# Optimization experiments

Hardware: AMD Instinct MI355X
Metric: run time of the kernel (lower is better)

## Reference

```python
import jax, jax.numpy as jnp
import numpy as np
import math

N, C, H = 2048, 256, 8
D = C // H
T, R, E = 8, 12, 32768
BUCKETS = 21
SEED = 128


def _layernorm(x, g, b, eps=1e-5):
    mu = jnp.mean(x, axis=-1, keepdims=True)
    var = jnp.var(x, axis=-1, keepdims=True)
    return (x - mu) * jax.lax.rsqrt(var + eps) * g + b


def _bucketize_dt(dt, num_buckets):
    eps = 1e-06
    signed_log = jnp.sign(dt) * jnp.log1p(jnp.abs(dt) + eps)
    min_v, max_v = -5.0, 5.0
    norm = (jnp.clip(signed_log, min_v, max_v) - min_v) / (max_v - min_v + 1e-09)
    idx = jnp.floor(norm * (num_buckets - 1)).astype(jnp.int32)
    return jnp.clip(idx, 0, num_buckets - 1)


def setup_inputs() -> dict:
    key = jax.random.key(0)
    ks = jax.random.split(key, 24)
    s = 0.02
    inp = {
        'X': jax.random.normal(ks[0], (N, C), jnp.float32),
        'token_type': jax.random.randint(ks[1], (N,), 0, T, jnp.int32),
        'edge_src': jax.random.randint(ks[2], (E,), 0, N, jnp.int32),
        'edge_dst': jax.random.randint(ks[3], (E,), 0, N, jnp.int32),
        'edge_rel': jax.random.randint(ks[4], (E,), 0, R, jnp.int32),
        'time_vec': jax.random.normal(ks[5], (N,), jnp.float32),
        'seed_count': SEED,
        'Wq': jax.random.normal(ks[6], (C, C), jnp.float32) * s,
        'bq': jnp.zeros((C,), jnp.float32),
        'Wk': jax.random.normal(ks[7], (C, C), jnp.float32) * s,
        'bk': jnp.zeros((C,), jnp.float32),
        'Wv': jax.random.normal(ks[8], (C, C), jnp.float32) * s,
        'bv': jnp.zeros((C,), jnp.float32),
        'Wo': jax.random.normal(ks[9], (C, C), jnp.float32) * s,
        'bo': jnp.zeros((C,), jnp.float32),
        'ln1_g': jnp.ones((C,), jnp.float32),
        'ln1_b': jnp.zeros((C,), jnp.float32),
        'ln2_g': jnp.ones((C,), jnp.float32),
        'ln2_b': jnp.zeros((C,), jnp.float32),
        'W1': jax.random.normal(ks[10], (C, 4 * C), jnp.float32) * s,
        'b1': jnp.zeros((4 * C,), jnp.float32),
        'W2': jax.random.normal(ks[11], (4 * C, C), jnp.float32) * s,
        'b2': jnp.zeros((C,), jnp.float32),
        'adj_rel_bias': jnp.zeros((R, H), jnp.float32),
        'typepair_bias': jnp.zeros((T, T, H), jnp.float32),
        'temp_bias': jax.random.normal(ks[12], (BUCKETS, H), jnp.float32) * s,
    }
    return inp


def reference(X, token_type, edge_src, edge_dst, edge_rel, time_vec, seed_count,
              Wq, bq, Wk, bk, Wv, bv, Wo, bo,
              ln1_g, ln1_b, ln2_g, ln2_b, W1, b1, W2, b2,
              adj_rel_bias, typepair_bias, temp_bias):
    n = X.shape[0]
    h = _layernorm(X, ln1_g, ln1_b)
    q = (h @ Wq + bq).reshape(n, H, D)
    k = (h @ Wk + bk).reshape(n, H, D)
    v = (h @ Wv + bv).reshape(n, H, D)
    scores = jnp.einsum('nhd,mhd->hnm', q, k) / math.sqrt(D)  # [H, N, N]

    # structural bias, factored as [N, N, H] then transposed
    bias = typepair_bias[token_type][:, token_type]            # [N, N, H]
    bias = bias.at[edge_src, edge_dst].add(adj_rel_bias[edge_rel])
    # seed-wise temporal bias on the first seed_count rows
    dt = time_vec[None, :] - time_vec[:seed_count, None]       # [S, N]
    tb = temp_bias[_bucketize_dt(dt, BUCKETS)]                 # [S, N, H]
    bias = bias.at[:seed_count].add(tb)

    attn = jax.nn.softmax(scores + bias.transpose(2, 0, 1), axis=-1)
    o = jnp.einsum('hnm,mhd->nhd', attn, v).reshape(n, C)
    x = X + (o @ Wo + bo)

    h2 = _layernorm(x, ln2_g, ln2_b)
    f = jax.nn.gelu(h2 @ W1 + b1, approximate=False) @ W2 + b2
    return x + f
```

## Files before the change

### kernel.cpp

```cpp
#include <hip/hip_runtime.h>
#include <hip/hip_bf16.h>
#include <math.h>

#define NTOK 2048
#define CDIM 256
#define HHEADS 8
#define DHEAD 32
#define NEDGE 32768
#define NTILE2 32
#define EXTD 64
#define LE 72
#define LP3 144

typedef __attribute__((ext_vector_type(8))) short short8;
typedef __attribute__((ext_vector_type(4))) short short4v;
typedef __attribute__((ext_vector_type(4))) float f32x4;

static __device__ inline short f2bf(float f) {
    __hip_bfloat16 h = __float2bfloat16(f);
    return *reinterpret_cast<short*>(&h);
}
static __device__ inline float bf2f(short s) {
    unsigned int u = ((unsigned int)(unsigned short)s) << 16;
    return *reinterpret_cast<float*>(&u);
}
static __device__ inline unsigned char f2fp8(float f) {
    int pk = __builtin_amdgcn_cvt_pk_fp8_f32(f, f, 0, false);
    return (unsigned char)(pk & 0xFF);
}

static __device__ inline void transpose_tile_f32(const float* __restrict__ in,
    short* __restrict__ out, int K, int N, int k0, int n0, int t)
{
    __shared__ float tile[64][65];
    int r0 = t >> 4, c0 = (t & 15) * 4;
    #pragma unroll
    for (int i = 0; i < 4; i++) {
        int r = r0 + i * 16;
        float4 v = *(const float4*)(in + (size_t)(k0 + r) * N + n0 + c0);
        tile[r][c0 + 0] = v.x; tile[r][c0 + 1] = v.y;
        tile[r][c0 + 2] = v.z; tile[r][c0 + 3] = v.w;
    }
    __syncthreads();
    #pragma unroll
    for (int i = 0; i < 4; i++) {
        int nr = r0 + i * 16;
        short o4[4];
        #pragma unroll
        for (int j = 0; j < 4; j++) o4[j] = f2bf(tile[c0 + j][nr]);
        *(short4v*)(out + (size_t)(n0 + nr) * K + k0 + c0) = *(short4v*)o4;
    }
}

__global__ __launch_bounds__(256) void prep_kernel(
    const float* __restrict__ Wq, const float* __restrict__ Wk,
    const float* __restrict__ Wv, const float* __restrict__ Wo,
    const float* __restrict__ W1, const float* __restrict__ W2,
    short* __restrict__ wt_qkv, short* __restrict__ wot,
    short* __restrict__ w1t, short* __restrict__ w2t,
    const int* __restrict__ token_type, const float* __restrict__ typepair_bias,
    short* __restrict__ qh, short* __restrict__ kh,
    int* __restrict__ cnt2, float* __restrict__ rowsum,
    const float* __restrict__ X, const float* __restrict__ ln1_g,
    const float* __restrict__ ln1_b, short* __restrict__ h1)
{
    int b = blockIdx.x;
    int t = threadIdx.x;
    if (b < 192) {
        const float* src; short* dst; int K, N, bx, by;
        if (b < 64) {
            int m = b >> 4, r = b & 15;
            src = (m == 0) ? Wq : (m == 1) ? Wk : (m == 2) ? Wv : Wo;
            dst = (m == 0) ? wt_qkv : (m == 1) ? wt_qkv + 256 * 256
                : (m == 2) ? wt_qkv + 512 * 256 : wot;
            K = 256; N = 256; bx = r & 3; by = r >> 2;
        } else if (b < 128) {
            int r = b - 64; src = W1; dst = w1t; K = 256; N = 1024; bx = r & 15; by = r >> 4;
        } else {
            int r = b - 128; src = W2; dst = w2t; K = 1024; N = 256; bx = r & 3; by = r >> 2;
        }
        transpose_tile_f32(src, dst, K, N, by * 64, bx * 64, t);
    } else if (b < 256) {
        int idx = (b - 192) * 256 + t;
        int row = idx >> 3, h = idx & 7;
        int tt = token_type[row];
        short qe[32], ke[32];
        #pragma unroll
        for (int j = 0; j < 32; j++) {
            if (j < 8) {
                qe[j] = f2bf(typepair_bias[(tt * 8 + j) * 8 + h]);
                ke[j] = (j == tt) ? (short)0x3F80 : (short)0;
            } else { qe[j] = 0; ke[j] = 0; }
        }
        size_t base = ((size_t)h * NTOK + row) * EXTD + 32;
        #pragma unroll
        for (int k = 0; k < 4; k++) {
            *(short8*)&qh[base + k * 8] = *(short8*)&qe[k * 8];
            *(short8*)&kh[base + k * 8] = *(short8*)&ke[k * 8];
        }
    } else if (b < 288) {
        int base = (b - 256) * 2048 + t * 8;
        #pragma unroll
        for (int i = 0; i < 8; i++) cnt2[base + i] = 0;
    } else if (b < 296) {
        int base = (b - 288) * 2048 + t * 8;
        #pragma unroll
        for (int i = 0; i < 8; i++) rowsum[base + i] = 0.0f;
    } else {
        int wv = t >> 6, lane = t & 63;
        int row = (b - 296) * 4 + wv;
        float4 x = *(const float4*)&X[(size_t)row * CDIM + lane * 4];
        float s = x.x + x.y + x.z + x.w;
        #pragma unroll
        for (int off = 1; off < 64; off <<= 1) s += __shfl_xor(s, off);
        float mu = s * (1.0f / CDIM);
        float4 d = { x.x - mu, x.y - mu, x.z - mu, x.w - mu };
        float s2 = d.x * d.x + d.y * d.y + d.z * d.z + d.w * d.w;
        #pragma unroll
        for (int off = 1; off < 64; off <<= 1) s2 += __shfl_xor(s2, off);
        float rsig = rsqrtf(s2 * (1.0f / CDIM) + 1e-5f);
        float4 gg = *(const float4*)&ln1_g[lane * 4];
        float4 bb = *(const float4*)&ln1_b[lane * 4];
        short o4[4];
        o4[0] = f2bf(d.x * rsig * gg.x + bb.x);
        o4[1] = f2bf(d.y * rsig * gg.y + bb.y);
        o4[2] = f2bf(d.z * rsig * gg.z + bb.z);
        o4[3] = f2bf(d.w * rsig * gg.w + bb.w);
        *(short4v*)&h1[(size_t)row * CDIM + lane * 4] = *(short4v*)o4;
    }
}

__global__ __launch_bounds__(256) void ln4_kernel(const float* __restrict__ X,
    const float* __restrict__ g, const float* __restrict__ b, short* __restrict__ out)
{
    int t = threadIdx.x;
    int wv = t >> 6, lane = t & 63;
    int row = blockIdx.x * 4 + wv;

    float4 x = *(const float4*)&X[(size_t)row * CDIM + lane * 4];
    float s = x.x + x.y + x.z + x.w;
    #pragma unroll
    for (int off = 1; off < 64; off <<= 1) s += __shfl_xor(s, off);
    float mu = s * (1.0f / CDIM);
    float4 d = { x.x - mu, x.y - mu, x.z - mu, x.w - mu };
    float s2 = d.x * d.x + d.y * d.y + d.z * d.z + d.w * d.w;
    #pragma unroll
    for (int off = 1; off < 64; off <<= 1) s2 += __shfl_xor(s2, off);
    float rsig = rsqrtf(s2 * (1.0f / CDIM) + 1e-5f);
    float4 gg = *(const float4*)&g[lane * 4];
    float4 bb = *(const float4*)&b[lane * 4];
    short o4[4];
    o4[0] = f2bf(d.x * rsig * gg.x + bb.x);
    o4[1] = f2bf(d.y * rsig * gg.y + bb.y);
    o4[2] = f2bf(d.z * rsig * gg.z + bb.z);
    o4[3] = f2bf(d.w * rsig * gg.w + bb.w);
    *(short4v*)&out[(size_t)row * CDIM + lane * 4] = *(short4v*)o4;
}

template<int EPI>
__global__ __launch_bounds__(256) void gemm32_kernel(
    const short* __restrict__ A, const short* __restrict__ Bt,
    const float* __restrict__ bias, const float* __restrict__ resid,
    void* __restrict__ out_, int M, int N, int K)
{
    __shared__ short A_lds[32 * 40];
    __shared__ short B_lds[64 * 40];

    const int t = threadIdx.x;
    const int w = t >> 6, lane = t & 63, c = lane & 15, g = lane >> 4;
    const int row0 = blockIdx.y * 32, col0 = blockIdx.x * 64;
    const int srow = t >> 2, sk = (t & 3) * 8;

    f32x4 acc[2] = {};

    for (int k0 = 0; k0 < K; k0 += 32) {
        if (t < 128)
            *(short8*)&A_lds[srow * 40 + sk] = *(const short8*)&A[(size_t)(row0 + srow) * K + k0 + sk];
        *(short8*)&B_lds[srow * 40 + sk] = *(const short8*)&Bt[(size_t)(col0 + srow) * K + k0 + sk];
        __syncthreads();
        short8 af = *(const short8*)&A_lds[((w & 1) * 16 + c) * 40 + g * 8];
        #pragma unroll
        for (int nf = 0; nf < 2; nf++) {
            short8 bf = *(const short8*)&B_lds[((w >> 1) * 32 + nf * 16 + c) * 40 + g * 8];
            acc[nf] = __builtin_amdgcn_mfma_f32_16x16x32_bf16(af, bf, acc[nf], 0, 0, 0);
        }
        __syncthreads();
    }

    #pragma unroll
    for (int nf = 0; nf < 2; nf++) {
        #pragma unroll
        for (int reg = 0; reg < 4; reg++) {
            int row = row0 + (w & 1) * 16 + g * 4 + reg;
            int col = col0 + (w >> 1) * 32 + nf * 16 + c;
            float v = acc[nf][reg] + bias[col];
            if (EPI == 2) {
                ((float*)out_)[(size_t)row * N + col] = v + resid[(size_t)row * N + col];
            } else {
                v = 0.5f * v * (1.0f + erff(v * 0.70710678118654752f));
                ((short*)out_)[(size_t)row * N + col] = f2bf(v);
            }
        }
    }
}

__global__ __launch_bounds__(256) void gemm32_qkv_kernel(
    const short* __restrict__ A, const short* __restrict__ Bt,
    const float* __restrict__ bq, const float* __restrict__ bk, const float* __restrict__ bv,
    short* __restrict__ qh, short* __restrict__ kh, unsigned char* __restrict__ vt8)
{
    const int K = CDIM;
    __shared__ short A_lds[32 * 40];
    __shared__ short B_lds[64 * 40];

    const int t = threadIdx.x;
    const int w = t >> 6, lane = t & 63, c = lane & 15, g = lane >> 4;
    const int row0 = blockIdx.y * 32, col0 = blockIdx.x * 64;
    const int srow = t >> 2, sk = (t & 3) * 8;

    f32x4 acc[2] = {};

    for (int k0 = 0; k0 < K; k0 += 32) {
        if (t < 128)
            *(short8*)&A_lds[srow * 40 + sk] = *(const short8*)&A[(size_t)(row0 + srow) * K + k0 + sk];
        *(short8*)&B_lds[srow * 40 + sk] = *(const short8*)&Bt[(size_t)(col0 + srow) * K + k0 + sk];
        __syncthreads();
        short8 af = *(const short8*)&A_lds[((w & 1) * 16 + c) * 40 + g * 8];
        #pragma unroll
        for (int nf = 0; nf < 2; nf++) {
            short8 bf = *(const short8*)&B_lds[((w >> 1) * 32 + nf * 16 + c) * 40 + g * 8];
            acc[nf] = __builtin_amdgcn_mfma_f32_16x16x32_bf16(af, bf, acc[nf], 0, 0, 0);
        }
        __syncthreads();
    }

    const int region = col0 >> 8;
    const int colr0 = col0 & 255;
    const float* bias = (region == 0) ? bq : (region == 1) ? bk : bv;
    #pragma unroll
    for (int nf = 0; nf < 2; nf++) {
        #pragma unroll
        for (int reg = 0; reg < 4; reg++) {
            int row = row0 + (w & 1) * 16 + g * 4 + reg;
            int col = colr0 + (w >> 1) * 32 + nf * 16 + c;
            float v = acc[nf][reg] + bias[col];
            if (region == 0) v *= 0.17677669529663687f;
            if (region < 2) {
                short bb = f2bf(v);
                size_t hidx = ((size_t)(col >> 5) * NTOK + row) * EXTD + (col & 31);
                if (region == 0) qh[hidx] = bb;
                else             kh[hidx] = bb;
            } else {
                int rl = row & 63;
                int rp = ((rl & 15) << 2) | (rl >> 4);
                vt8[(size_t)col * NTOK + (row & ~63) + rp] = f2fp8(v);
            }
        }
    }
}

__global__ void edge_hist2_kernel(const int* __restrict__ src, const int* __restrict__ dst,
    int* __restrict__ cnt, int E)
{
    int e = blockIdx.x * blockDim.x + threadIdx.x;
    if (e < E) atomicAdd(&cnt[src[e] * NTILE2 + (dst[e] >> 6)], 1);
}

__global__ __launch_bounds__(256) void edge_scan2_kernel(const int* __restrict__ cnt,
    int* __restrict__ row_ptr, int* __restrict__ wcur)
{
    __shared__ int sums[256];
    int t = threadIdx.x;
    int base = t * 256;
    int s = 0;
    for (int i = 0; i < 64; i++) {
        int4 v = *(const int4*)&cnt[base + i * 4];
        s += v.x + v.y + v.z + v.w;
    }
    sums[t] = s;
    __syncthreads();
    for (int off = 1; off < 256; off <<= 1) {
        int v = (t >= off) ? sums[t - off] : 0;
        __syncthreads();
        sums[t] += v;
        __syncthreads();
    }
    int run = (t == 0) ? 0 : sums[t - 1];
    for (int i = 0; i < 64; i++) {
        int4 v = *(const int4*)&cnt[base + i * 4];
        int4 o;
        o.x = run; run += v.x;
        o.y = run; run += v.y;
        o.z = run; run += v.z;
        o.w = run; run += v.w;
        *(int4*)&row_ptr[base + i * 4] = o;
        *(int4*)&wcur[base + i * 4] = o;
    }
    if (t == 255) row_ptr[NTOK * NTILE2] = run;
}

__global__ void edge_scatter2_kernel(const int* __restrict__ src, const int* __restrict__ dst,
    const int* __restrict__ rel, int* __restrict__ wcur, int2* __restrict__ pairs, int E)
{
    int e = blockIdx.x * blockDim.x + threadIdx.x;
    if (e < E) {
        int d = dst[e];
        int pos = atomicAdd(&wcur[src[e] * NTILE2 + (d >> 6)], 1);
        pairs[pos] = make_int2(d, rel[e]);
    }
}

__global__ __launch_bounds__(256) void sgemm_exp_kernel(
    const short* __restrict__ qh, const short* __restrict__ kh,
    const float* __restrict__ time_vec, const int* __restrict__ seed_ptr,
    const float* __restrict__ adj_rel_bias, const float* __restrict__ temp_bias,
    const int* __restrict__ row_ptr2, const int2* __restrict__ pairs2,
    unsigned char* __restrict__ S8, float* __restrict__ rowsum)
{
    __shared__ short A_lds[64 * LE];
    __shared__ short B_lds[64 * LE];
    __shared__ float tcol_s[64];
    __shared__ float temp_h[21];
    __shared__ float adj_h[12];
    __shared__ int rpA[64], rpB[64];

    const int t = threadIdx.x;
    const int w = t >> 6, lane = t & 63, c = lane & 15, g = lane >> 4;
    const int h = blockIdx.z;
    const int m0 = blockIdx.x * 64, n0 = blockIdx.y * 64;
    const int seed = seed_ptr[0];

    {
        int r = t >> 3, off = (t & 7) * 8;
        *(short8*)&A_lds[r * LE + off] =
            *(const short8*)&qh[((size_t)h * NTOK + n0 + r) * EXTD + off];
        *(short8*)&A_lds[(r + 32) * LE + off] =
            *(const short8*)&qh[((size_t)h * NTOK + n0 + 32 + r) * EXTD + off];
        *(short8*)&B_lds[r * LE + off] =
            *(const short8*)&kh[((size_t)h * NTOK + m0 + r) * EXTD + off];
        *(short8*)&B_lds[(r + 32) * LE + off] =
            *(const short8*)&kh[((size_t)h * NTOK + m0 + 32 + r) * EXTD + off];
    }
    if (t < 64) {
        tcol_s[t] = time_vec[m0 + t];
        int bidx = (n0 + t) * NTILE2 + (m0 >> 6);
        rpA[t] = row_ptr2[bidx];
        rpB[t] = row_ptr2[bidx + 1];
    }
    if (t < 21) temp_h[t] = temp_bias[t * HHEADS + h];
    if (t < 12) adj_h[t] = adj_rel_bias[t * HHEADS + h];
    __syncthreads();

    short8 alo = *(const short8*)&A_lds[(w * 16 + c) * LE + g * 8];
    short8 ahi = *(const short8*)&A_lds[(w * 16 + c) * LE + 32 + g * 8];
    f32x4 acc[4] = {};
    #pragma unroll
    for (int nf = 0; nf < 4; nf++) {
        short8 blo = *(const short8*)&B_lds[(nf * 16 + c) * LE + g * 8];
        short8 bhi = *(const short8*)&B_lds[(nf * 16 + c) * LE + 32 + g * 8];
        acc[nf] = __builtin_amdgcn_mfma_f32_16x16x32_bf16(alo, blo, acc[nf], 0, 0, 0);
        acc[nf] = __builtin_amdgcn_mfma_f32_16x16x32_bf16(ahi, bhi, acc[nf], 0, 0, 0);
    }

    #pragma unroll
    for (int reg = 0; reg < 4; reg++) {
        const int rloc = w * 16 + g * 4 + reg;
        const int n = n0 + rloc;
        const bool rowTemp = (n < seed);
        const float tn = rowTemp ? time_vec[n] : 0.0f;

        {
            int e0 = rpA[rloc], e1 = rpB[rloc];
            for (int e = e0; e < e1; ++e) {
                int2 pr = pairs2[e];
                int cl = pr.x & 63;
                if ((cl & 15) == c) {
                    float ab = adj_h[pr.y];
                    int nfi = cl >> 4;
                    #pragma unroll
                    for (int nf = 0; nf < 4; nf++)
                        if (nf == nfi) acc[nf][reg] += ab;
                }
            }
        }

        float rsum = 0.0f;
        float ev[4];
        #pragma unroll
        for (int nf = 0; nf < 4; nf++) {
            float s = acc[nf][reg];
            if (rowTemp) {
                float dt = tcol_s[nf * 16 + c] - tn;
                float ab = fabsf(dt) + 1e-6f;
                float sg = (dt > 0.0f) ? 1.0f : ((dt < 0.0f) ? -1.0f : 0.0f);
                float sl = sg * log1pf(ab);
                sl = fminf(fmaxf(sl, -5.0f), 5.0f);
                float norm = (sl + 5.0f) * (1.0f / (10.0f + 1e-9f));
                int bidx = (int)floorf(norm * 20.0f);
                bidx = min(max(bidx, 0), 20);
                s += temp_h[bidx];
            }
            float e = __expf(s);
            rsum += e;
            ev[nf] = e;
        }
        int lo = __builtin_amdgcn_cvt_pk_fp8_f32(ev[0], ev[1], 0, false);
        int hi = __builtin_amdgcn_cvt_pk_fp8_f32(ev[2], ev[3], 0, false);
        unsigned word = ((unsigned)lo & 0xFFFFu) | ((unsigned)hi << 16);
        *(unsigned*)&S8[((size_t)h * NTOK + n) * NTOK + m0 + c * 4] = word;
        rsum += __shfl_xor(rsum, 1);
        rsum += __shfl_xor(rsum, 2);
        rsum += __shfl_xor(rsum, 4);
        rsum += __shfl_xor(rsum, 8);
        if (c == 0) atomicAdd(&rowsum[h * NTOK + n], rsum);
    }
}

__global__ __launch_bounds__(256) void pv_kernel(
    const unsigned char* __restrict__ P8, const unsigned char* __restrict__ vt8,
    const float* __restrict__ rowsum, short* __restrict__ o)
{
    __shared__ __align__(16) unsigned char A_lds[32 * LP3];
    __shared__ __align__(16) unsigned char B_lds[32 * LP3];
    const int t = threadIdx.x;
    const int w = t >> 6, lane = t & 63, c = lane & 15, g = lane >> 4;
    const int h = blockIdx.y;
    const int n0 = blockIdx.x * 32;
    const int rowblk = (w & 1) * 16, colblk = (w >> 1) * 16;

    f32x4 acc = {0.0f, 0.0f, 0.0f, 0.0f};

    for (int k0 = 0; k0 < NTOK; k0 += 128) {
        int r = t >> 3, off = (t & 7) * 16;
        *(int4*)&A_lds[r * LP3 + off] =
            *(const int4*)&P8[((size_t)h * NTOK + n0 + r) * NTOK + k0 + off];
        *(int4*)&B_lds[r * LP3 + off] =
            *(const int4*)&vt8[(size_t)(h * 32 + r) * NTOK + k0 + off];
        __syncthreads();
        #pragma unroll
        for (int kk = 0; kk < 4; kk++) {
            long long a = *(const long long*)&A_lds[(rowblk + c) * LP3 + kk * 32 + g * 8];
            long long b = *(const long long*)&B_lds[(colblk + c) * LP3 + kk * 32 + g * 8];
            acc = __builtin_amdgcn_mfma_f32_16x16x32_fp8_fp8(a, b, acc, 0, 0, 0);
        }
        __syncthreads();
    }

    #pragma unroll
    for (int reg = 0; reg < 4; reg++) {
        int row = n0 + rowblk + g * 4 + reg;
        int col = h * 32 + colblk + c;
        float inv = 1.0f / rowsum[h * NTOK + row];
        o[(size_t)row * CDIM + col] = f2bf(acc[reg] * inv);
    }
}

extern "C" void kernel_launch(void* const* d_in, const int* in_sizes, int n_in,
                              void* d_out, int out_size, void* d_ws, size_t ws_size,
                              hipStream_t stream)
{
    (void)in_sizes; (void)n_in; (void)out_size; (void)ws_size;
    const float* X        = (const float*)d_in[0];
    const int* token_type = (const int*)d_in[1];
    const int* edge_src   = (const int*)d_in[2];
    const int* edge_dst   = (const int*)d_in[3];
    const int* edge_rel   = (const int*)d_in[4];
    const float* time_vec = (const float*)d_in[5];
    const int* seed_ptr   = (const int*)d_in[6];
    const float* Wq = (const float*)d_in[7];  const float* bq = (const float*)d_in[8];
    const float* Wk = (const float*)d_in[9];  const float* bk = (const float*)d_in[10];
    const float* Wv = (const float*)d_in[11]; const float* bv = (const float*)d_in[12];
    const float* Wo = (const float*)d_in[13]; const float* bo = (const float*)d_in[14];
    const float* ln1_g = (const float*)d_in[15]; const float* ln1_b = (const float*)d_in[16];
    const float* ln2_g = (const float*)d_in[17]; const float* ln2_b = (const float*)d_in[18];
    const float* W1 = (const float*)d_in[19]; const float* b1 = (const float*)d_in[20];
    const float* W2 = (const float*)d_in[21]; const float* b2 = (const float*)d_in[22];
    const float* adj_rel_bias  = (const float*)d_in[23];
    const float* typepair_bias = (const float*)d_in[24];
    const float* temp_bias     = (const float*)d_in[25];
    float* out = (float*)d_out;

    char* base = (char*)d_ws;
    size_t off = 0;
    auto alloc = [&](size_t bytes) { char* p = base + off; off += (bytes + 255) & ~(size_t)255; return p; };
    short* qh_bf   = (short*)alloc((size_t)HHEADS * NTOK * EXTD * 2);
    short* kh_bf   = (short*)alloc((size_t)HHEADS * NTOK * EXTD * 2);
    unsigned char* vt8 = (unsigned char*)alloc((size_t)256 * NTOK);
    short* h1_bf   = (short*)alloc((size_t)NTOK * 256 * 2);
    short* h2_bf   = (short*)alloc((size_t)NTOK * 256 * 2);
    short* o_bf    = (short*)alloc((size_t)NTOK * 256 * 2);
    short* mid_bf  = (short*)alloc((size_t)NTOK * 1024 * 2);
    float* xb      = (float*)alloc((size_t)NTOK * 256 * 4);
    short* wt_qkv  = (short*)alloc((size_t)768 * 256 * 2);
    short* wot     = (short*)alloc((size_t)256 * 256 * 2);
    short* w1t     = (short*)alloc((size_t)1024 * 256 * 2);
    short* w2t     = (short*)alloc((size_t)256 * 1024 * 2);
    int2*  pairs2  = (int2*)alloc((size_t)NEDGE * 8);
    int*   cnt2    = (int*)alloc((size_t)NTOK * NTILE2 * 4);
    int*   rowptr2 = (int*)alloc(((size_t)NTOK * NTILE2 + 4) * 4);
    int*   wcur2   = (int*)alloc((size_t)NTOK * NTILE2 * 4);
    float* rowsum  = (float*)alloc((size_t)HHEADS * NTOK * 4);
    unsigned char* S8 = (unsigned char*)alloc((size_t)HHEADS * NTOK * NTOK);

    prep_kernel<<<808, 256, 0, stream>>>(Wq, Wk, Wv, Wo, W1, W2,
                                         wt_qkv, wot, w1t, w2t,
                                         token_type, typepair_bias,
                                         qh_bf, kh_bf, cnt2, rowsum,
                                         X, ln1_g, ln1_b, h1_bf);

    edge_hist2_kernel<<<NEDGE / 256, 256, 0, stream>>>(edge_src, edge_dst, cnt2, NEDGE);
    edge_scan2_kernel<<<1, 256, 0, stream>>>(cnt2, rowptr2, wcur2);
    edge_scatter2_kernel<<<NEDGE / 256, 256, 0, stream>>>(edge_src, edge_dst, edge_rel, wcur2, pairs2, NEDGE);

    gemm32_qkv_kernel<<<dim3(12, 64), 256, 0, stream>>>(h1_bf, wt_qkv, bq, bk, bv,
                                                        qh_bf, kh_bf, vt8);

    sgemm_exp_kernel<<<dim3(32, 32, 8), 256, 0, stream>>>(
        qh_bf, kh_bf, time_vec, seed_ptr, adj_rel_bias, temp_bias,
        rowptr2, pairs2, S8, rowsum);
    pv_kernel<<<dim3(64, 8), 256, 0, stream>>>(S8, vt8, rowsum, o_bf);

    gemm32_kernel<2><<<dim3(4, 64), 256, 0, stream>>>(o_bf, wot, bo, X, xb, NTOK, 256, 256);

    ln4_kernel<<<NTOK / 4, 256, 0, stream>>>(xb, ln2_g, ln2_b, h2_bf);

    gemm32_kernel<3><<<dim3(16, 64), 256, 0, stream>>>(h2_bf, w1t, b1, nullptr, mid_bf, NTOK, 1024, 256);
    gemm32_kernel<2><<<dim3(4, 64), 256, 0, stream>>>(mid_bf, w2t, b2, xb, out, NTOK, 256, 1024);
}
```

Before: 146.0 us.

## Compute softmax row sums via MFMA in PV kernel, drop atomics

The exp kernel no longer accumulates row sums with shuffles and global atomics. The PV kernel instead runs a second fp8 MFMA against a ones vector (0x38 is 1.0 in e4m3) to sum the fp8-quantized probabilities it actually consumes. The zeroing pass for the rowsum buffer is removed, and each exp block now handles two 64-column tiles, which halves the grid and reuses the Q tile. This doubles the MFMA work in the PV loop and serialises two K tiles per block behind an extra barrier.

```diff
diff --git a/kernel.cpp b/kernel.cpp
--- a/kernel.cpp
+++ b/kernel.cpp
@@ -60,7 +60,7 @@
     short* __restrict__ w1t, short* __restrict__ w2t,
     const int* __restrict__ token_type, const float* __restrict__ typepair_bias,
     short* __restrict__ qh, short* __restrict__ kh,
-    int* __restrict__ cnt2, float* __restrict__ rowsum,
+    int* __restrict__ cnt2,
     const float* __restrict__ X, const float* __restrict__ ln1_g,
     const float* __restrict__ ln1_b, short* __restrict__ h1)
 {
@@ -102,13 +102,9 @@
         int base = (b - 256) * 2048 + t * 8;
         #pragma unroll
         for (int i = 0; i < 8; i++) cnt2[base + i] = 0;
-    } else if (b < 296) {
-        int base = (b - 288) * 2048 + t * 8;
-        #pragma unroll
-        for (int i = 0; i < 8; i++) rowsum[base + i] = 0.0f;
     } else {
         int wv = t >> 6, lane = t & 63;
-        int row = (b - 296) * 4 + wv;
+        int row = (b - 288) * 4 + wv;
         float4 x = *(const float4*)&X[(size_t)row * CDIM + lane * 4];
         float s = x.x + x.y + x.z + x.w;
         #pragma unroll
@@ -315,7 +311,7 @@
     const float* __restrict__ time_vec, const int* __restrict__ seed_ptr,
     const float* __restrict__ adj_rel_bias, const float* __restrict__ temp_bias,
     const int* __restrict__ row_ptr2, const int2* __restrict__ pairs2,
-    unsigned char* __restrict__ S8, float* __restrict__ rowsum)
+    unsigned char* __restrict__ S8)
 {
     __shared__ short A_lds[64 * LE];
     __shared__ short B_lds[64 * LE];
@@ -327,7 +323,7 @@
     const int t = threadIdx.x;
     const int w = t >> 6, lane = t & 63, c = lane & 15, g = lane >> 4;
     const int h = blockIdx.z;
-    const int m0 = blockIdx.x * 64, n0 = blockIdx.y * 64;
+    const int m_base = blockIdx.x * 128, n0 = blockIdx.y * 64;
     const int seed = seed_ptr[0];
 
     {
@@ -336,89 +332,90 @@
             *(const short8*)&qh[((size_t)h * NTOK + n0 + r) * EXTD + off];
         *(short8*)&A_lds[(r + 32) * LE + off] =
             *(const short8*)&qh[((size_t)h * NTOK + n0 + 32 + r) * EXTD + off];
-        *(short8*)&B_lds[r * LE + off] =
-            *(const short8*)&kh[((size_t)h * NTOK + m0 + r) * EXTD + off];
-        *(short8*)&B_lds[(r + 32) * LE + off] =
-            *(const short8*)&kh[((size_t)h * NTOK + m0 + 32 + r) * EXTD + off];
-    }
-    if (t < 64) {
-        tcol_s[t] = time_vec[m0 + t];
-        int bidx = (n0 + t) * NTILE2 + (m0 >> 6);
-        rpA[t] = row_ptr2[bidx];
-        rpB[t] = row_ptr2[bidx + 1];
     }
     if (t < 21) temp_h[t] = temp_bias[t * HHEADS + h];
     if (t < 12) adj_h[t] = adj_rel_bias[t * HHEADS + h];
-    __syncthreads();
-
-    short8 alo = *(const short8*)&A_lds[(w * 16 + c) * LE + g * 8];
-    short8 ahi = *(const short8*)&A_lds[(w * 16 + c) * LE + 32 + g * 8];
-    f32x4 acc[4] = {};
-    #pragma unroll
-    for (int nf = 0; nf < 4; nf++) {
-        short8 blo = *(const short8*)&B_lds[(nf * 16 + c) * LE + g * 8];
-        short8 bhi = *(const short8*)&B_lds[(nf * 16 + c) * LE + 32 + g * 8];
-        acc[nf] = __builtin_amdgcn_mfma_f32_16x16x32_bf16(alo, blo, acc[nf], 0, 0, 0);
-        acc[nf] = __builtin_amdgcn_mfma_f32_16x16x32_bf16(ahi, bhi, acc[nf], 0, 0, 0);
-    }
-
-    #pragma unroll
-    for (int reg = 0; reg < 4; reg++) {
-        const int rloc = w * 16 + g * 4 + reg;
-        const int n = n0 + rloc;
-        const bool rowTemp = (n < seed);
-        const float tn = rowTemp ? time_vec[n] : 0.0f;
-
+
+    #pragma unroll
+    for (int mi = 0; mi < 2; mi++) {
+        const int m0 = m_base + mi * 64;
+        if (mi) __syncthreads();
         {
-            int e0 = rpA[rloc], e1 = rpB[rloc];
-            for (int e = e0; e < e1; ++e) {
-                int2 pr = pairs2[e];
-                int cl = pr.x & 63;
-                if ((cl & 15) == c) {
-                    float ab = adj_h[pr.y];
-                    int nfi = cl >> 4;
-                    #pragma unroll
-                    for (int nf = 0; nf < 4; nf++)
-                        if (nf == nfi) acc[nf][reg] += ab;
+            int r = t >> 3, off = (t & 7) * 8;
+            *(short8*)&B_lds[r * LE + off] =
+                *(const short8*)&kh[((size_t)h * NTOK + m0 + r) * EXTD + off];
+            *(short8*)&B_lds[(r + 32) * LE + off] =
+                *(const short8*)&kh[((size_t)h * NTOK + m0 + 32 + r) * EXTD + off];
+        }
+        if (t < 64) {
+            tcol_s[t] = time_vec[m0 + t];
+            int bidx = (n0 + t) * NTILE2 + (m0 >> 6);
+            rpA[t] = row_ptr2[bidx];
+            rpB[t] = row_ptr2[bidx + 1];
+        }
+        __syncthreads();
+
+        short8 alo = *(const short8*)&A_lds[(w * 16 + c) * LE + g * 8];
+        short8 ahi = *(const short8*)&A_lds[(w * 16 + c) * LE + 32 + g * 8];
+        f32x4 acc[4] = {};
+        #pragma unroll
+        for (int nf = 0; nf < 4; nf++) {
+            short8 blo = *(const short8*)&B_lds[(nf * 16 + c) * LE + g * 8];
+            short8 bhi = *(const short8*)&B_lds[(nf * 16 + c) * LE + 32 + g * 8];
+            acc[nf] = __builtin_amdgcn_mfma_f32_16x16x32_bf16(alo, blo, acc[nf], 0, 0, 0);
+            acc[nf] = __builtin_amdgcn_mfma_f32_16x16x32_bf16(ahi, bhi, acc[nf], 0, 0, 0);
+        }
+
+        #pragma unroll
+        for (int reg = 0; reg < 4; reg++) {
+            const int rloc = w * 16 + g * 4 + reg;
+            const int n = n0 + rloc;
+            const bool rowTemp = (n < seed);
+            const float tn = rowTemp ? time_vec[n] : 0.0f;
+
+            {
+                int e0 = rpA[rloc], e1 = rpB[rloc];
+                for (int e = e0; e < e1; ++e) {
+                    int2 pr = pairs2[e];
+                    int cl = pr.x & 63;
+                    if ((cl & 15) == c) {
+                        float ab = adj_h[pr.y];
+                        int nfi = cl >> 4;
+                        #pragma unroll
+                        for (int nf = 0; nf < 4; nf++)
+                            if (nf == nfi) acc[nf][reg] += ab;
+                    }
                 }
             }
-        }
-
-        float rsum = 0.0f;
-        float ev[4];
-        #pragma unroll
-        for (int nf = 0; nf < 4; nf++) {
-            float s = acc[nf][reg];
-            if (rowTemp) {
-                float dt = tcol_s[nf * 16 + c] - tn;
-                float ab = fabsf(dt) + 1e-6f;
-                float sg = (dt > 0.0f) ? 1.0f : ((dt < 0.0f) ? -1.0f : 0.0f);
-                float sl = sg * log1pf(ab);
-                sl = fminf(fmaxf(sl, -5.0f), 5.0f);
-                float norm = (sl + 5.0f) * (1.0f / (10.0f + 1e-9f));
-                int bidx = (int)floorf(norm * 20.0f);
-                bidx = min(max(bidx, 0), 20);
-                s += temp_h[bidx];
+
+            float ev[4];
+            #pragma unroll
+            for (int nf = 0; nf < 4; nf++) {
+                float s = acc[nf][reg];
+                if (rowTemp) {
+                    float dt = tcol_s[nf * 16 + c] - tn;
+                    float ab = fabsf(dt) + 1e-6f;
+                    float sg = (dt > 0.0f) ? 1.0f : ((dt < 0.0f) ? -1.0f : 0.0f);
+                    float sl = sg * log1pf(ab);
+                    sl = fminf(fmaxf(sl, -5.0f), 5.0f);
+                    float norm = (sl + 5.0f) * (1.0f / (10.0f + 1e-9f));
+                    int bidx = (int)floorf(norm * 20.0f);
+                    bidx = min(max(bidx, 0), 20);
+                    s += temp_h[bidx];
+                }
+                ev[nf] = __expf(s);
             }
-            float e = __expf(s);
-            rsum += e;
-            ev[nf] = e;
-        }
-        int lo = __builtin_amdgcn_cvt_pk_fp8_f32(ev[0], ev[1], 0, false);
-        int hi = __builtin_amdgcn_cvt_pk_fp8_f32(ev[2], ev[3], 0, false);
-        unsigned word = ((unsigned)lo & 0xFFFFu) | ((unsigned)hi << 16);
-        *(unsigned*)&S8[((size_t)h * NTOK + n) * NTOK + m0 + c * 4] = word;
-        rsum += __shfl_xor(rsum, 1);
-        rsum += __shfl_xor(rsum, 2);
-        rsum += __shfl_xor(rsum, 4);
-        rsum += __shfl_xor(rsum, 8);
-        if (c == 0) atomicAdd(&rowsum[h * NTOK + n], rsum);
+            int lo = __builtin_amdgcn_cvt_pk_fp8_f32(ev[0], ev[1], 0, false);
+            int hi = __builtin_amdgcn_cvt_pk_fp8_f32(ev[2], ev[3], 0, false);
+            unsigned word = ((unsigned)lo & 0xFFFFu) | ((unsigned)hi << 16);
+            *(unsigned*)&S8[((size_t)h * NTOK + n) * NTOK + m0 + c * 4] = word;
+        }
     }
 }
 
 __global__ __launch_bounds__(256) void pv_kernel(
     const unsigned char* __restrict__ P8, const unsigned char* __restrict__ vt8,
-    const float* __restrict__ rowsum, short* __restrict__ o)
+    short* __restrict__ o)
 {
     __shared__ __align__(16) unsigned char A_lds[32 * LP3];
     __shared__ __align__(16) unsigned char B_lds[32 * LP3];
@@ -427,8 +424,10 @@
     const int h = blockIdx.y;
     const int n0 = blockIdx.x * 32;
     const int rowblk = (w & 1) * 16, colblk = (w >> 1) * 16;
-
-    f32x4 acc = {0.0f, 0.0f, 0.0f, 0.0f};
+    const long long ones8 = 0x3838383838383838LL;
+
+    f32x4 acc  = {0.0f, 0.0f, 0.0f, 0.0f};
+    f32x4 accs = {0.0f, 0.0f, 0.0f, 0.0f};
 
     for (int k0 = 0; k0 < NTOK; k0 += 128) {
         int r = t >> 3, off = (t & 7) * 16;
@@ -441,7 +440,8 @@
         for (int kk = 0; kk < 4; kk++) {
             long long a = *(const long long*)&A_lds[(rowblk + c) * LP3 + kk * 32 + g * 8];
             long long b = *(const long long*)&B_lds[(colblk + c) * LP3 + kk * 32 + g * 8];
-            acc = __builtin_amdgcn_mfma_f32_16x16x32_fp8_fp8(a, b, acc, 0, 0, 0);
+            acc  = __builtin_amdgcn_mfma_f32_16x16x32_fp8_fp8(a, b, acc, 0, 0, 0);
+            accs = __builtin_amdgcn_mfma_f32_16x16x32_fp8_fp8(a, ones8, accs, 0, 0, 0);
         }
         __syncthreads();
     }
@@ -450,7 +450,7 @@
     for (int reg = 0; reg < 4; reg++) {
         int row = n0 + rowblk + g * 4 + reg;
         int col = h * 32 + colblk + c;
-        float inv = 1.0f / rowsum[h * NTOK + row];
+        float inv = 1.0f / accs[reg];
         o[(size_t)row * CDIM + col] = f2bf(acc[reg] * inv);
     }
 }
@@ -499,13 +499,12 @@
     int*   cnt2    = (int*)alloc((size_t)NTOK * NTILE2 * 4);
     int*   rowptr2 = (int*)alloc(((size_t)NTOK * NTILE2 + 4) * 4);
     int*   wcur2   = (int*)alloc((size_t)NTOK * NTILE2 * 4);
-    float* rowsum  = (float*)alloc((size_t)HHEADS * NTOK * 4);
     unsigned char* S8 = (unsigned char*)alloc((size_t)HHEADS * NTOK * NTOK);
 
-    prep_kernel<<<808, 256, 0, stream>>>(Wq, Wk, Wv, Wo, W1, W2,
+    prep_kernel<<<800, 256, 0, stream>>>(Wq, Wk, Wv, Wo, W1, W2,
                                          wt_qkv, wot, w1t, w2t,
                                          token_type, typepair_bias,
-                                         qh_bf, kh_bf, cnt2, rowsum,
+                                         qh_bf, kh_bf, cnt2,
                                          X, ln1_g, ln1_b, h1_bf);
 
     edge_hist2_kernel<<<NEDGE / 256, 256, 0, stream>>>(edge_src, edge_dst, cnt2, NEDGE);
@@ -515,10 +514,10 @@
     gemm32_qkv_kernel<<<dim3(12, 64), 256, 0, stream>>>(h1_bf, wt_qkv, bq, bk, bv,
                                                         qh_bf, kh_bf, vt8);
 
-    sgemm_exp_kernel<<<dim3(32, 32, 8), 256, 0, stream>>>(
+    sgemm_exp_kernel<<<dim3(16, 32, 8), 256, 0, stream>>>(
         qh_bf, kh_bf, time_vec, seed_ptr, adj_rel_bias, temp_bias,
-        rowptr2, pairs2, S8, rowsum);
-    pv_kernel<<<dim3(64, 8), 256, 0, stream>>>(S8, vt8, rowsum, o_bf);
+        rowptr2, pairs2, S8);
+    pv_kernel<<<dim3(64, 8), 256, 0, stream>>>(S8, vt8, o_bf);
 
     gemm32_kernel<2><<<dim3(4, 64), 256, 0, stream>>>(o_bf, wot, bo, X, xb, NTOK, 256, 256);
 
```

Result: no change. 147.0 us (+0.7%).
